# Kernel optimization log

Measured on AMD Instinct MI355X. Metric: run time of the kernel, lower is better.

Reference implementation:

```python
import jax, jax.numpy as jnp
import numpy as np

B, S, E, H = 4, 1024, 1024, 16
HD = E // H


def setup_inputs() -> dict:
    key = jax.random.key(0)
    ks = jax.random.split(key, 5)
    x = jax.random.normal(ks[0], (B, S, E), dtype=jnp.float32)
    # causal mask: True = masked (filled with -inf), as in masked_fill_
    mask = jnp.triu(jnp.ones((S, S), dtype=bool), k=1)
    in_proj_weight = jax.random.normal(ks[1], (3 * E, E), dtype=jnp.float32) * (E ** -0.5)
    in_proj_bias = jax.random.normal(ks[2], (3 * E,), dtype=jnp.float32) * 0.02
    out_w = jax.random.normal(ks[3], (E, E), dtype=jnp.float32) * (E ** -0.5)
    out_b = jax.random.normal(ks[4], (E,), dtype=jnp.float32) * 0.02
    return {"x": x, "mask": mask, "in_proj_weight": in_proj_weight,
            "in_proj_bias": in_proj_bias, "out_w": out_w, "out_b": out_b}


def reference(x, mask, in_proj_weight, in_proj_bias, out_w, out_b):
    scaling = HD ** -0.5
    # fused QKV projection (self-attention path: qkv_same)
    qkv = jnp.einsum('bse,fe->bsf', x, in_proj_weight) + in_proj_bias  # [B,S,3E]
    q, k, v = jnp.split(qkv, 3, axis=-1)
    # split heads -> [B,H,S,HD]
    def heads(t):
        return t.reshape(B, S, H, HD).transpose(0, 2, 1, 3)
    q, k, v = heads(q), heads(k), heads(v)
    scores = jnp.einsum('bhsd,bhtd->bhst', q, k) * scaling  # [B,H,S,S]
    scores = jnp.where(mask[None, None, :, :], -jnp.inf, scores)
    att = jax.nn.softmax(scores, axis=-1)  # dropout p=0.0 (eval)
    out = jnp.einsum('bhst,bhtd->bhsd', att, v)  # [B,H,S,HD]
    out = out.transpose(0, 2, 1, 3).reshape(B, S, E)  # concat heads
    out = jnp.einsum('bse,fe->bsf', out, out_w) + out_b
    att_weights = att.reshape(B * H, S, S)
    return out, att_weights
```

## Files before the change

### kernel.cpp

```cpp
#include <hip/hip_runtime.h>
#include <hip/hip_bf16.h>
#include <stdint.h>

#define NH 16
#define SEQ 1024
#define EMB 1024
#define HDIM 64
#define BATCH 4
#define SPAD 1032

typedef float f32x4 __attribute__((ext_vector_type(4)));
typedef short bf16x8 __attribute__((ext_vector_type(8)));

static __device__ __forceinline__ short f2bf(float f) {
  union { float f; uint32_t u; } v; v.f = f;
  uint32_t r = (v.u + 0x7FFF + ((v.u >> 16) & 1)) >> 16;
  return (short)(uint16_t)r;
}
static __device__ __forceinline__ float bf2f(short h) {
  union { uint32_t u; float f; } v; v.u = ((uint32_t)(uint16_t)h) << 16;
  return v.f;
}

static __device__ __forceinline__ void gload_lds16(const void* g, void* l) {
  __builtin_amdgcn_global_load_lds(
      (const __attribute__((address_space(1))) void*)g,
      (__attribute__((address_space(3))) void*)l, 16, 0, 0);
}

static __device__ __forceinline__ void cvt8(const float* s, short* d) {
  const float4* sv = (const float4*)s;
  float4 a = sv[0], b = sv[1];
  bf16x8 o;
  o[0] = f2bf(a.x); o[1] = f2bf(a.y); o[2] = f2bf(a.z); o[3] = f2bf(a.w);
  o[4] = f2bf(b.x); o[5] = f2bf(b.y); o[6] = f2bf(b.z); o[7] = f2bf(b.w);
  *(bf16x8*)d = o;
}

__global__ void cvt3_kernel(const float* __restrict__ x, const float* __restrict__ w,
                            const float* __restrict__ o, short* __restrict__ xb,
                            short* __restrict__ wb, short* __restrict__ ob) {
  int i = (blockIdx.x * blockDim.x + threadIdx.x) * 8;
  if (i < 4194304) {
    cvt8(x + i, xb + i);
  } else if (i < 7340032) {
    cvt8(w + (i - 4194304), wb + (i - 4194304));
  } else {
    cvt8(o + (i - 7340032), ob + (i - 7340032));
  }
}

__global__ __launch_bounds__(256) void transpose_v(const short* __restrict__ v,
                                                   short* __restrict__ vt) {
  __shared__ short t[64][72];
  const int tid = threadIdx.x;
  const int bh = blockIdx.y;
  const int sb = blockIdx.x * 64;
  const int row = tid >> 2;
  const int c0 = (tid & 3) * 16;
  const short* src = v + ((size_t)(bh * SEQ + sb + row)) * HDIM + c0;
  *(bf16x8*)&t[row][c0] = *(const bf16x8*)src;
  *(bf16x8*)&t[row][c0 + 8] = *(const bf16x8*)(src + 8);
  __syncthreads();
  bf16x8 o0, o1;
#pragma unroll
  for (int i = 0; i < 8; ++i) o0[i] = t[c0 + i][row];
#pragma unroll
  for (int i = 0; i < 8; ++i) o1[i] = t[c0 + 8 + i][row];
  short* dst = vt + ((size_t)(bh * HDIM + row)) * SEQ + sb + c0;
  *(bf16x8*)dst = o0;
  *(bf16x8*)(dst + 8) = o1;
}

#define STAGE_QKV(bb, kk0)                                                     \
  {                                                                            \
    _Pragma("unroll") for (int c = 0; c < 2; ++c) {                            \
      int oo = o + c * 1024;                                                   \
      int row = oo >> 6;                                                       \
      int scol = (oo & 63) ^ ((row & 3) << 4);                                 \
      gload_lds16((const char*)A + ((size_t)(row0 + row) * K + (kk0)) * 2 + scol, \
                  (char*)As[bb] + (w * 2 + c) * 1024);                         \
      gload_lds16((const char*)Bm + ((size_t)(col0 + row) * K + (kk0)) * 2 + scol,\
                  (char*)Bs[bb] + (w * 2 + c) * 1024);                         \
    }                                                                          \
  }

#define COMPUTE_QKV(bb)                                                        \
  {                                                                            \
    bf16x8 af[4], bfr[4];                                                      \
    const int kbo = (l4 * 16) ^ ((l15 & 3) << 4);                              \
    _Pragma("unroll") for (int i = 0; i < 4; ++i) {                            \
      af[i] = *(const bf16x8*)((const char*)As[bb] + (wr * 64 + i * 16 + l15) * 64 + kbo); \
      bfr[i] = *(const bf16x8*)((const char*)Bs[bb] + (wc * 64 + i * 16 + l15) * 64 + kbo); \
    }                                                                          \
    _Pragma("unroll") for (int i = 0; i < 4; ++i)                              \
      _Pragma("unroll") for (int j = 0; j < 4; ++j)                            \
        acc[i][j] = __builtin_amdgcn_mfma_f32_16x16x32_bf16(af[i], bfr[j], acc[i][j], 0, 0, 0); \
  }

__global__ __launch_bounds__(256) void gemm_qkv(
    const short* __restrict__ A, const short* __restrict__ Bm,
    const float* __restrict__ bias, short* __restrict__ qkvws) {
  __shared__ short As[2][128 * 32];
  __shared__ short Bs[2][128 * 32];
  const int tid = threadIdx.x;
  const int w = tid >> 6, l = tid & 63;
  const int l15 = l & 15, l4 = l >> 4;
  const int wr = w >> 1, wc = w & 1;
  const int row0 = blockIdx.x * 128;
  const int col0 = blockIdx.y * 128;
  const int K = EMB;

  f32x4 acc[4][4] = {};

  const int o = (w * 2) * 1024 + l * 16;
  STAGE_QKV(0, 0);
  __syncthreads();

  int cur = 0;
  for (int k0 = 0; k0 < K; k0 += 32) {
    if (k0 + 32 < K) STAGE_QKV(cur ^ 1, k0 + 32);
    COMPUTE_QKV(cur);
    __syncthreads();
    cur ^= 1;
  }

#pragma unroll
  for (int j = 0; j < 4; ++j) {
    int f = col0 + wc * 64 + j * 16 + l15;
    float bv = bias[f];
    int part = f >> 10;
    int e = f & 1023;
    int hh = e >> 6, d = e & 63;
#pragma unroll
    for (int i = 0; i < 4; ++i) {
#pragma unroll
      for (int rr = 0; rr < 4; ++rr) {
        int m = row0 + wr * 64 + i * 16 + l4 * 4 + rr;
        int bb = m >> 10, ss = m & 1023;
        qkvws[(size_t)part * 4194304 +
              ((size_t)(bb * NH + hh) * SEQ + ss) * HDIM + d] =
            f2bf(acc[i][j][rr] + bv);
      }
    }
  }
}

#define STAGE_OUT(bb, kk0)                                                     \
  {                                                                            \
    _Pragma("unroll") for (int c = 0; c < 2; ++c) {                            \
      int oo = oA + c * 1024;                                                  \
      int row = oo >> 6;                                                       \
      int scol = (oo & 63) ^ ((row & 3) << 4);                                 \
      gload_lds16((const char*)A + ((size_t)(row0 + row) * K + (kk0)) * 2 + scol, \
                  (char*)As[bb] + (w * 2 + c) * 1024);                         \
    }                                                                          \
    {                                                                          \
      int oo = oB;                                                             \
      int row = oo >> 6;                                                       \
      int scol = (oo & 63) ^ ((row & 3) << 4);                                 \
      gload_lds16((const char*)Bm + ((size_t)(col0 + row) * K + (kk0)) * 2 + scol,\
                  (char*)Bs[bb] + w * 1024);                                   \
    }                                                                          \
  }

#define COMPUTE_OUT(bb)                                                        \
  {                                                                            \
    bf16x8 af[2], bfr[4];                                                      \
    const int kbo = (l4 * 16) ^ ((l15 & 3) << 4);                              \
    _Pragma("unroll") for (int i = 0; i < 2; ++i)                              \
      af[i] = *(const bf16x8*)((const char*)As[bb] + (w * 32 + i * 16 + l15) * 64 + kbo); \
    _Pragma("unroll") for (int j = 0; j < 4; ++j)                              \
      bfr[j] = *(const bf16x8*)((const char*)Bs[bb] + (j * 16 + l15) * 64 + kbo); \
    _Pragma("unroll") for (int i = 0; i < 2; ++i)                              \
      _Pragma("unroll") for (int j = 0; j < 4; ++j)                            \
        acc[i][j] = __builtin_amdgcn_mfma_f32_16x16x32_bf16(af[i], bfr[j], acc[i][j], 0, 0, 0); \
  }

__global__ __launch_bounds__(256) void gemm_out64(
    const short* __restrict__ A, const short* __restrict__ Bm,
    const float* __restrict__ bias, float* __restrict__ outp) {
  __shared__ short As[2][128 * 32];
  __shared__ short Bs[2][64 * 32];
  const int tid = threadIdx.x;
  const int w = tid >> 6, l = tid & 63;
  const int l15 = l & 15, l4 = l >> 4;
  const int row0 = blockIdx.x * 128;
  const int col0 = blockIdx.y * 64;
  const int K = EMB;

  f32x4 acc[2][4] = {};

  const int oA = (w * 2) * 1024 + l * 16;
  const int oB = w * 1024 + l * 16;
  STAGE_OUT(0, 0);
  __syncthreads();

  int cur = 0;
  for (int k0 = 0; k0 < K; k0 += 32) {
    if (k0 + 32 < K) STAGE_OUT(cur ^ 1, k0 + 32);
    COMPUTE_OUT(cur);
    __syncthreads();
    cur ^= 1;
  }

#pragma unroll
  for (int j = 0; j < 4; ++j) {
    int f = col0 + j * 16 + l15;
    float bv = bias[f];
#pragma unroll
    for (int i = 0; i < 2; ++i)
#pragma unroll
      for (int rr = 0; rr < 4; ++rr) {
        int m = row0 + w * 32 + i * 16 + l4 * 4 + rr;
        __builtin_nontemporal_store(acc[i][j][rr] + bv, &outp[(size_t)m * EMB + f]);
      }
  }
}

__global__ __launch_bounds__(256) void attn_kernel(
    const short* __restrict__ qws, const short* __restrict__ kws,
    const short* __restrict__ vtws, float* __restrict__ attg,
    short* __restrict__ aow) {
  __shared__ short strip[32 * SPAD];
  __shared__ float wsum[4][32];
  __shared__ float inv_sum[32];

  const int tid = threadIdx.x;
  const int w = tid >> 6, l = tid & 63;
  const int l15 = l & 15, l4 = l >> 4;
  const int blk = blockIdx.x;
  const int bh = blk >> 5;
  const int r = blk & 31;
  const int rowbase = r * 32;

  const short* qb = qws + ((size_t)bh * SEQ + rowbase) * HDIM;
  const short* kb = kws + (size_t)bh * SEQ * HDIM;
  const short* vb = vtws + (size_t)bh * HDIM * SEQ;

  bf16x8 qf[2][2];
#pragma unroll
  for (int rg = 0; rg < 2; ++rg)
#pragma unroll
    for (int ks = 0; ks < 2; ++ks)
      qf[rg][ks] = *(const bf16x8*)(qb + (rg * 16 + l15) * HDIM + ks * 32 + l4 * 8);

  const int ngroups = (rowbase + 32) >> 4;
  float psum[2][4] = {};

  for (int g = w; g < ngroups; g += 4) {
    const short* kg = kb + (g * 16 + l15) * HDIM + l4 * 8;
    bf16x8 kf0 = *(const bf16x8*)(kg);
    bf16x8 kf1 = *(const bf16x8*)(kg + 32);
    f32x4 a0 = {}, a1 = {};
    a0 = __builtin_amdgcn_mfma_f32_16x16x32_bf16(qf[0][0], kf0, a0, 0, 0, 0);
    a0 = __builtin_amdgcn_mfma_f32_16x16x32_bf16(qf[0][1], kf1, a0, 0, 0, 0);
    a1 = __builtin_amdgcn_mfma_f32_16x16x32_bf16(qf[1][0], kf0, a1, 0, 0, 0);
    a1 = __builtin_amdgcn_mfma_f32_16x16x32_bf16(qf[1][1], kf1, a1, 0, 0, 0);
    int col = g * 16 + l15;
#pragma unroll
    for (int rg = 0; rg < 2; ++rg) {
#pragma unroll
      for (int rr = 0; rr < 4; ++rr) {
        int rloc = rg * 16 + l4 * 4 + rr;
        int row = rowbase + rloc;
        float sv = (rg ? a1[rr] : a0[rr]) * 0.125f;
        float ev = (col <= row) ? __expf(sv) : 0.0f;
        psum[rg][rr] += ev;
        strip[rloc * SPAD + col] = f2bf(ev);
      }
    }
  }

#pragma unroll
  for (int rg = 0; rg < 2; ++rg)
#pragma unroll
    for (int rr = 0; rr < 4; ++rr) {
      float v = psum[rg][rr];
      v += __shfl_xor(v, 1);
      v += __shfl_xor(v, 2);
      v += __shfl_xor(v, 4);
      v += __shfl_xor(v, 8);
      psum[rg][rr] = v;
    }
  if (l15 == 0) {
#pragma unroll
    for (int rg = 0; rg < 2; ++rg)
#pragma unroll
      for (int rr = 0; rr < 4; ++rr)
        wsum[w][rg * 16 + l4 * 4 + rr] = psum[rg][rr];
  }
  __syncthreads();
  if (tid < 32) {
    float s = wsum[0][tid] + wsum[1][tid] + wsum[2][tid] + wsum[3][tid];
    inv_sum[tid] = 1.0f / s;
  }
  __syncthreads();

  {
    const int limit = ngroups * 16;
    const int rloc = tid >> 3;
    const int cb = tid & 7;
    float* arow = attg + (size_t)bh * SEQ * SEQ + (size_t)(rowbase + rloc) * SEQ;
    float isr = inv_sum[rloc];
#pragma unroll
    for (int i = 0; i < 16; ++i) {
      int c = (cb + i * 8) * 8;
      f32x4 o0, o1;
      if (c < limit) {
        bf16x8 p = *(const bf16x8*)&strip[rloc * SPAD + c];
        o0[0] = bf2f(p[0]) * isr; o0[1] = bf2f(p[1]) * isr;
        o0[2] = bf2f(p[2]) * isr; o0[3] = bf2f(p[3]) * isr;
        o1[0] = bf2f(p[4]) * isr; o1[1] = bf2f(p[5]) * isr;
        o1[2] = bf2f(p[6]) * isr; o1[3] = bf2f(p[7]) * isr;
      } else {
        o0 = (f32x4)0.0f;
        o1 = (f32x4)0.0f;
      }
      __builtin_nontemporal_store(o0, (f32x4*)(arow + c));
      __builtin_nontemporal_store(o1, (f32x4*)(arow + c + 4));
    }
  }

  {
    const int nch = ngroups >> 1;
    const int d0 = w * 16;
    f32x4 oacc[2] = {};
    const short* vrow = vb + (d0 + l15) * SEQ + l4 * 8;
    for (int c = 0; c < nch; ++c) {
      bf16x8 vf = *(const bf16x8*)(vrow + c * 32);
      bf16x8 p0 = *(const bf16x8*)&strip[(0 + l15) * SPAD + c * 32 + l4 * 8];
      bf16x8 p1 = *(const bf16x8*)&strip[(16 + l15) * SPAD + c * 32 + l4 * 8];
      oacc[0] = __builtin_amdgcn_mfma_f32_16x16x32_bf16(p0, vf, oacc[0], 0, 0, 0);
      oacc[1] = __builtin_amdgcn_mfma_f32_16x16x32_bf16(p1, vf, oacc[1], 0, 0, 0);
    }
    const int b = bh >> 4, h = bh & 15;
#pragma unroll
    for (int rg = 0; rg < 2; ++rg) {
#pragma unroll
      for (int rr = 0; rr < 4; ++rr) {
        int rloc = rg * 16 + l4 * 4 + rr;
        int s = rowbase + rloc;
        float v = oacc[rg][rr] * inv_sum[rloc];
        aow[((size_t)(b * SEQ + s)) * EMB + h * HDIM + d0 + l15] = f2bf(v);
      }
    }
  }
}

extern "C" void kernel_launch(void* const* d_in, const int* in_sizes, int n_in,
                              void* d_out, int out_size, void* d_ws, size_t ws_size,
                              hipStream_t stream) {
  (void)in_sizes; (void)n_in; (void)out_size; (void)ws_size;
  const float* x = (const float*)d_in[0];
  const float* ipw = (const float*)d_in[2];
  const float* ipb = (const float*)d_in[3];
  const float* ow = (const float*)d_in[4];
  const float* ob = (const float*)d_in[5];
  float* outp = (float*)d_out;
  float* attg = (float*)d_out + (size_t)BATCH * SEQ * EMB;

  char* ws = (char*)d_ws;
  short* xbf = (short*)(ws);
  short* wbf = (short*)(ws + 8388608);
  short* owbf = (short*)(ws + 14680064);
  short* qkvws = (short*)(ws + 16777216);
  short* aow = (short*)(ws + 41943040);
  short* vtws = (short*)(ws);

  short* qws = qkvws;
  short* kws = qkvws + 4194304;
  short* vws = qkvws + 8388608;

  cvt3_kernel<<<4096, 256, 0, stream>>>(x, ipw, ow, xbf, wbf, owbf);

  dim3 g1(32, 24);
  gemm_qkv<<<g1, 256, 0, stream>>>(xbf, wbf, ipb, qkvws);

  transpose_v<<<dim3(16, 64), 256, 0, stream>>>(vws, vtws);

  attn_kernel<<<2048, 256, 0, stream>>>(qws, kws, vtws, attg, aow);

  gemm_out64<<<dim3(32, 16), 256, 0, stream>>>(aow, owbf, ob, outp);
}
```

Measured before the change: 177.5 us.

## Rewrite QKV GEMM as 256x256 tile with 4-stage async LDS pipeline

The QKV projection GEMM moves from 128x128 tiles with 256 threads and double buffering to 256x256 tiles with 512 threads (8 waves, each computing 128x64) and a 4-deep ring of LDS buffers. Loads are issued three stages ahead, with explicit vmcnt waits and raw s_barrier calls, and the MFMA block runs at raised wave priority. The aim is better data reuse per tile and more latency hiding for global loads. In exchange it uses much more LDS (128 KB per block), so occupancy per CU drops, and the grid shrinks to 192 blocks, which could under-fill the device.

```diff
diff --git a/kernel.cpp b/kernel.cpp
--- a/kernel.cpp
+++ b/kernel.cpp
@@ -72,58 +72,76 @@
   *(bf16x8*)(dst + 8) = o1;
 }
 
-#define STAGE_QKV(bb, kk0)                                                     \
+#define STAGEK(bb, kk0)                                                        \
   {                                                                            \
-    _Pragma("unroll") for (int c = 0; c < 2; ++c) {                            \
-      int oo = o + c * 1024;                                                   \
-      int row = oo >> 6;                                                       \
-      int scol = (oo & 63) ^ ((row & 3) << 4);                                 \
-      gload_lds16((const char*)A + ((size_t)(row0 + row) * K + (kk0)) * 2 + scol, \
-                  (char*)As[bb] + (w * 2 + c) * 1024);                         \
-      gload_lds16((const char*)Bm + ((size_t)(col0 + row) * K + (kk0)) * 2 + scol,\
-                  (char*)Bs[bb] + (w * 2 + c) * 1024);                         \
+    int oo0 = w * 2048 + l * 16;                                               \
+    int r0 = oo0 >> 6; int sc0 = (oo0 & 63) ^ ((r0 & 3) << 4);                 \
+    int oo1 = oo0 + 1024;                                                      \
+    int r1 = oo1 >> 6; int sc1 = (oo1 & 63) ^ ((r1 & 3) << 4);                 \
+    gload_lds16((const char*)A + ((size_t)(row0 + r0) * K + (kk0)) * 2 + sc0,  \
+                (char*)&As[(bb) * 8192] + w * 2048);                           \
+    gload_lds16((const char*)A + ((size_t)(row0 + r1) * K + (kk0)) * 2 + sc1,  \
+                (char*)&As[(bb) * 8192] + w * 2048 + 1024);                    \
+    gload_lds16((const char*)Bm + ((size_t)(col0 + r0) * K + (kk0)) * 2 + sc0, \
+                (char*)&Bs[(bb) * 8192] + w * 2048);                           \
+    gload_lds16((const char*)Bm + ((size_t)(col0 + r1) * K + (kk0)) * 2 + sc1, \
+                (char*)&Bs[(bb) * 8192] + w * 2048 + 1024);                    \
+  }
+
+#define KT(bb, DOSTAGE, t3, WAITN)                                             \
+  {                                                                            \
+    asm volatile("s_waitcnt vmcnt(" #WAITN ")" ::: "memory");                  \
+    __builtin_amdgcn_s_barrier();                                              \
+    asm volatile("" ::: "memory");                                             \
+    bf16x8 af[8], bfr[4];                                                      \
+    const short* Ab = &As[(bb) * 8192];                                        \
+    const short* Bb = &Bs[(bb) * 8192];                                        \
+    _Pragma("unroll") for (int i = 0; i < 8; ++i) {                            \
+      int r = wr * 128 + i * 16 + l15;                                         \
+      af[i] = *(const bf16x8*)((const char*)Ab + r * 64 +                      \
+                               ((l4 * 16) ^ ((r & 3) << 4)));                  \
     }                                                                          \
-  }
-
-#define COMPUTE_QKV(bb)                                                        \
-  {                                                                            \
-    bf16x8 af[4], bfr[4];                                                      \
-    const int kbo = (l4 * 16) ^ ((l15 & 3) << 4);                              \
-    _Pragma("unroll") for (int i = 0; i < 4; ++i) {                            \
-      af[i] = *(const bf16x8*)((const char*)As[bb] + (wr * 64 + i * 16 + l15) * 64 + kbo); \
-      bfr[i] = *(const bf16x8*)((const char*)Bs[bb] + (wc * 64 + i * 16 + l15) * 64 + kbo); \
+    _Pragma("unroll") for (int j = 0; j < 4; ++j) {                            \
+      int r = wc * 64 + j * 16 + l15;                                          \
+      bfr[j] = *(const bf16x8*)((const char*)Bb + r * 64 +                     \
+                                ((l4 * 16) ^ ((r & 3) << 4)));                 \
     }                                                                          \
-    _Pragma("unroll") for (int i = 0; i < 4; ++i)                              \
+    if (DOSTAGE) { STAGEK((t3) & 3, (t3) * 32); }                              \
+    asm volatile("s_waitcnt lgkmcnt(0)" ::: "memory");                         \
+    __builtin_amdgcn_sched_barrier(0);                                         \
+    __builtin_amdgcn_s_setprio(1);                                             \
+    _Pragma("unroll") for (int i = 0; i < 8; ++i)                              \
       _Pragma("unroll") for (int j = 0; j < 4; ++j)                            \
-        acc[i][j] = __builtin_amdgcn_mfma_f32_16x16x32_bf16(af[i], bfr[j], acc[i][j], 0, 0, 0); \
-  }
-
-__global__ __launch_bounds__(256) void gemm_qkv(
+        acc[i][j] = __builtin_amdgcn_mfma_f32_16x16x32_bf16(af[i], bfr[j],     \
+                                                            acc[i][j], 0, 0, 0); \
+    __builtin_amdgcn_s_setprio(0);                                             \
+  }
+
+__global__ __launch_bounds__(512, 2) void gemm_qkv8(
     const short* __restrict__ A, const short* __restrict__ Bm,
     const float* __restrict__ bias, short* __restrict__ qkvws) {
-  __shared__ short As[2][128 * 32];
-  __shared__ short Bs[2][128 * 32];
+  __shared__ short As[4 * 8192];
+  __shared__ short Bs[4 * 8192];
   const int tid = threadIdx.x;
   const int w = tid >> 6, l = tid & 63;
   const int l15 = l & 15, l4 = l >> 4;
-  const int wr = w >> 1, wc = w & 1;
-  const int row0 = blockIdx.x * 128;
-  const int col0 = blockIdx.y * 128;
+  const int wr = w >> 2, wc = w & 3;
+  const int row0 = blockIdx.x * 256;
+  const int col0 = blockIdx.y * 256;
   const int K = EMB;
 
-  f32x4 acc[4][4] = {};
-
-  const int o = (w * 2) * 1024 + l * 16;
-  STAGE_QKV(0, 0);
-  __syncthreads();
-
-  int cur = 0;
-  for (int k0 = 0; k0 < K; k0 += 32) {
-    if (k0 + 32 < K) STAGE_QKV(cur ^ 1, k0 + 32);
-    COMPUTE_QKV(cur);
-    __syncthreads();
-    cur ^= 1;
-  }
+  f32x4 acc[8][4] = {};
+
+  STAGEK(0, 0);
+  STAGEK(1, 32);
+  STAGEK(2, 64);
+
+  for (int t = 0; t < 29; ++t) {
+    KT(t & 3, 1, t + 3, 8);
+  }
+  KT(1, 0, 0, 8);
+  KT(2, 0, 0, 4);
+  KT(3, 0, 0, 0);
 
 #pragma unroll
   for (int j = 0; j < 4; ++j) {
@@ -133,14 +151,14 @@
     int e = f & 1023;
     int hh = e >> 6, d = e & 63;
 #pragma unroll
-    for (int i = 0; i < 4; ++i) {
+    for (int mi = 0; mi < 8; ++mi) {
 #pragma unroll
       for (int rr = 0; rr < 4; ++rr) {
-        int m = row0 + wr * 64 + i * 16 + l4 * 4 + rr;
-        int bb = m >> 10, ss = m & 1023;
+        int m = row0 + wr * 128 + mi * 16 + l4 * 4 + rr;
+        int bb2 = m >> 10, ss = m & 1023;
         qkvws[(size_t)part * 4194304 +
-              ((size_t)(bb * NH + hh) * SEQ + ss) * HDIM + d] =
-            f2bf(acc[i][j][rr] + bv);
+              ((size_t)(bb2 * NH + hh) * SEQ + ss) * HDIM + d] =
+            f2bf(acc[mi][j][rr] + bv);
       }
     }
   }
@@ -374,8 +392,8 @@
 
   cvt3_kernel<<<4096, 256, 0, stream>>>(x, ipw, ow, xbf, wbf, owbf);
 
-  dim3 g1(32, 24);
-  gemm_qkv<<<g1, 256, 0, stream>>>(xbf, wbf, ipb, qkvws);
+  dim3 g1(16, 12);
+  gemm_qkv8<<<g1, 512, 0, stream>>>(xbf, wbf, ipb, qkvws);
 
   transpose_v<<<dim3(16, 64), 256, 0, stream>>>(vws, vtws);
 
```

Result: slower. 181.7 us (+2.4%).
